# Kernel optimization log

Hardware: AMD Instinct MI355X
Metric: run time of the kernel (lower is better)

The kernel has to match this reference:

```python
import jax, jax.numpy as jnp
import numpy as np

EPSILON = 0.01  # from init_kwargs

def setup_inputs() -> dict:
    key = jax.random.key(0)
    k1, k2, k3, k4 = jax.random.split(key, 4)
    N, E, D = 100000, 3200000, 4
    x = jax.random.normal(k1, (N, D), dtype=jnp.float32)
    edge_index = jax.random.randint(k2, (2, E), 0, N, dtype=jnp.int32)
    boo_values = jax.random.normal(k3, (E, D, D), dtype=jnp.float32)
    mask = jnp.ones((N, 1), dtype=jnp.float32)
    diag = jax.random.uniform(k4, (N, D), dtype=jnp.float32)
    return {"x": x, "edge_index": edge_index, "boo_values": boo_values,
            "mask": mask, "diag": diag}

def reference(x, edge_index, boo_values, mask, diag):
    # y = eps*diag*x + A @ (diag * (A^T @ x)), A blocked-sparse with
    # per-edge blocks A_{row,col} = boo_values[e] in R^{DxD}.
    N = x.shape[0]
    row, col = edge_index[0], edge_index[1]
    # spmv_t (A^T x): gather x at row i, message A_ij^T x_i, scatter-add to col j
    msg_t = jnp.einsum('eji,ej->ei', boo_values, x[row])  # [E, D]
    AT_x = jax.ops.segment_sum(msg_t, col, num_segments=N) * mask  # [N, D]
    eps_x = EPSILON * x
    AT_x = AT_x * diag
    eps_x = eps_x * diag
    # spmv (A v): gather v at col j, message A_ij v_j, scatter-add to row i
    msg = jnp.einsum('eij,ej->ei', boo_values, AT_x[col])  # [E, D]
    A_AT_x = jax.ops.segment_sum(msg, row, num_segments=N) * mask  # [N, D]
    return eps_x + A_AT_x
```

## Files before the change

### kernel.cpp

```cpp
#include <hip/hip_runtime.h>

#define EPSILON 0.01f

#define BLK    256
#define SLICE  1024
#define SLOG   10
#define PCH    20
#define BCH    2048
#define MAXS   128


__global__ void init_cursors(int* cur1, int* cur2, int S, int cap) {
    int t = threadIdx.x;
    if (t < S) { cur1[t] = t * cap; cur2[t] = t * cap; }
}

__global__ void __launch_bounds__(BLK) bin_kernel(
    const int* __restrict__ row, const int* __restrict__ col,
    int2* __restrict__ bins1, int2* __restrict__ bins2,
    int* __restrict__ cur1, int* __restrict__ cur2,
    long long E, int S)
{
    __shared__ int2 st[BCH];
    __shared__ unsigned char ss[BCH];
    __shared__ int hist[MAXS], rnk[MAXS], sbase[MAXS], gbase[MAXS];
    const int t = threadIdx.x;

    long long start = (long long)blockIdx.x * BCH;
    long long endl  = start + BCH; if (endl > E) endl = E;
    const int cnt = (int)(endl - start);

    for (int side = 0; side < 2; ++side) {
        const int* __restrict__ key = side ? row : col;
        const int* __restrict__ oth = side ? col : row;
        int2* __restrict__ bins = side ? bins2 : bins1;
        int*  __restrict__ cur  = side ? cur2  : cur1;

        if (t < MAXS) { hist[t] = 0; rnk[t] = 0; }
        __syncthreads();

        for (int i0 = t * 4; i0 < cnt; i0 += BLK * 4) {
            if (i0 + 4 <= cnt) {
                int4 k = *reinterpret_cast<const int4*>(key + start + i0);
                atomicAdd(&hist[k.x >> SLOG], 1);
                atomicAdd(&hist[k.y >> SLOG], 1);
                atomicAdd(&hist[k.z >> SLOG], 1);
                atomicAdd(&hist[k.w >> SLOG], 1);
            } else {
                for (int i = i0; i < cnt; ++i)
                    atomicAdd(&hist[key[start + i] >> SLOG], 1);
            }
        }
        __syncthreads();

        if (t == 0) {
            int run = 0;
            for (int s2 = 0; s2 < S; ++s2) { sbase[s2] = run; run += hist[s2]; }
        }
        if (t < S) gbase[t] = atomicAdd(&cur[t], hist[t]);
        __syncthreads();

        for (int i0 = t * 4; i0 < cnt; i0 += BLK * 4) {
            if (i0 + 4 <= cnt) {
                int4 k = *reinterpret_cast<const int4*>(key + start + i0);
                int4 o = *reinterpret_cast<const int4*>(oth + start + i0);
                int kk[4] = {k.x, k.y, k.z, k.w};
                int oo[4] = {o.x, o.y, o.z, o.w};
                #pragma unroll
                for (int u = 0; u < 4; ++u) {
                    int s2 = kk[u] >> SLOG;
                    int slot = sbase[s2] + atomicAdd(&rnk[s2], 1);
                    st[slot] = make_int2((int)(start + i0 + u),
                                         ((kk[u] & (SLICE - 1)) << 17) | oo[u]);
                    ss[slot] = (unsigned char)s2;
                }
            } else {
                for (int i = i0; i < cnt; ++i) {
                    int kv = key[start + i], ov = oth[start + i];
                    int s2 = kv >> SLOG;
                    int slot = sbase[s2] + atomicAdd(&rnk[s2], 1);
                    st[slot] = make_int2((int)(start + i),
                                         ((kv & (SLICE - 1)) << 17) | ov);
                    ss[slot] = (unsigned char)s2;
                }
            }
        }
        __syncthreads();

        for (int i = t; i < cnt; i += BLK) {
            int s2 = ss[i];
            bins[(size_t)gbase[s2] + (i - sbase[s2])] = st[i];
        }
        __syncthreads();
    }
}

template<int PASS>
__global__ void __launch_bounds__(BLK) pass_kernel(
    const float4* __restrict__ boo,
    const int2*   __restrict__ bins,
    const int*    __restrict__ cur,
    const float4* __restrict__ src,
    float*        __restrict__ stage,
    int N, int cap, int P)
{
    __shared__ float acc[SLICE * 4];

    const int s    = blockIdx.x / P;
    const int p    = blockIdx.x - s * P;
    const int base = s << SLOG;
    const int lim  = min(SLICE, N - base);

    for (int i = threadIdx.x; i < SLICE * 4; i += BLK) acc[i] = 0.0f;
    __syncthreads();

    const int cnt = cur[s] - s * cap;
    const int lo  = (int)((long long)cnt * p / P);
    const int hi  = (int)((long long)cnt * (p + 1) / P);
    const int2* __restrict__ bin = bins + (size_t)s * cap;

    const int j  = (int)(threadIdx.x & 3);
    const int g0 = (int)(threadIdx.x >> 2);

    auto process = [&](int2 rec, float4 b) {
        float4 v = src[rec.y & 0x1FFFF];
        int loc = ((unsigned)rec.y) >> 17;
        float val;
        if (PASS == 2) {
            val = b.x * v.x + b.y * v.y + b.z * v.z + b.w * v.w;
        } else {
            float xj = (j == 0) ? v.x : (j == 1) ? v.y : (j == 2) ? v.z : v.w;
            float4 q;
            q.x = b.x * xj; q.y = b.y * xj; q.z = b.z * xj; q.w = b.w * xj;
            q.x += __shfl_xor(q.x, 1); q.y += __shfl_xor(q.y, 1);
            q.z += __shfl_xor(q.z, 1); q.w += __shfl_xor(q.w, 1);
            q.x += __shfl_xor(q.x, 2); q.y += __shfl_xor(q.y, 2);
            q.z += __shfl_xor(q.z, 2); q.w += __shfl_xor(q.w, 2);
            val = (j == 0) ? q.x : (j == 1) ? q.y : (j == 2) ? q.z : q.w;
        }
        atomicAdd(&acc[loc * 4 + j], val);
    };

    int i = lo + g0;
    for (; i + 64 < hi; i += 128) {
        int2 ra = bin[i];
        int2 rb = bin[i + 64];
        float4 ba = boo[(long long)ra.x * 4 + j];
        float4 bb = boo[(long long)rb.x * 4 + j];
        process(ra, ba);
        process(rb, bb);
    }
    if (i < hi) {
        int2 ra = bin[i];
        float4 ba = boo[(long long)ra.x * 4 + j];
        process(ra, ba);
    }
    __syncthreads();

    float* stg = stage + (size_t)blockIdx.x * (SLICE * 4);
    for (int f = threadIdx.x; f < lim * 4; f += BLK) stg[f] = acc[f];
}

__global__ void __launch_bounds__(BLK) mid_staged_kernel(
    const float4* __restrict__ stage,
    const float4* __restrict__ d4,
    const float*  __restrict__ mask,
    float4* __restrict__ v4,
    int N, int P)
{
    int n = blockIdx.x * BLK + threadIdx.x;
    if (n >= N) return;
    int s = n >> SLOG, local = n & (SLICE - 1);
    const float4* t = stage + ((size_t)s * P) * SLICE + local;
    float4 a = make_float4(0.f, 0.f, 0.f, 0.f);
    for (int p = 0; p < P; ++p) {
        float4 u = t[(size_t)p * SLICE];
        a.x += u.x; a.y += u.y; a.z += u.z; a.w += u.w;
    }
    float4 dv = d4[n];
    float  m  = mask[n];
    a.x *= dv.x * m; a.y *= dv.y * m; a.z *= dv.z * m; a.w *= dv.w * m;
    v4[n] = a;
}

__global__ void __launch_bounds__(BLK) fin_staged_kernel(
    const float4* __restrict__ stage,
    const float4* __restrict__ x4,
    const float4* __restrict__ d4,
    const float*  __restrict__ mask,
    float4* __restrict__ out4,
    int N, int P)
{
    int n = blockIdx.x * BLK + threadIdx.x;
    if (n >= N) return;
    int s = n >> SLOG, local = n & (SLICE - 1);
    const float4* t = stage + ((size_t)s * P) * SLICE + local;
    float4 a = make_float4(0.f, 0.f, 0.f, 0.f);
    for (int p = 0; p < P; ++p) {
        float4 u = t[(size_t)p * SLICE];
        a.x += u.x; a.y += u.y; a.z += u.z; a.w += u.w;
    }
    float4 xv = x4[n];
    float4 dv = d4[n];
    float  m  = mask[n];
    float4 o;
    o.x = EPSILON * xv.x * dv.x + a.x * m;
    o.y = EPSILON * xv.y * dv.y + a.y * m;
    o.z = EPSILON * xv.z * dv.z + a.z * m;
    o.w = EPSILON * xv.w * dv.w + a.w * m;
    out4[n] = o;
}

__global__ void __launch_bounds__(BLK) mid_atomic_kernel(
    const float4* __restrict__ x4,
    const float4* __restrict__ d4,
    const float*  __restrict__ mask,
    float4* __restrict__ atx,
    float4* __restrict__ out4,
    int N)
{
    int n = blockIdx.x * BLK + threadIdx.x;
    if (n >= N) return;
    float4 a  = atx[n];
    float4 dv = d4[n];
    float  m  = mask[n];
    a.x *= dv.x * m; a.y *= dv.y * m; a.z *= dv.z * m; a.w *= dv.w * m;
    atx[n] = a;
    float4 xv = x4[n];
    float4 o;
    o.x = EPSILON * xv.x * dv.x; o.y = EPSILON * xv.y * dv.y;
    o.z = EPSILON * xv.z * dv.z; o.w = EPSILON * xv.w * dv.w;
    out4[n] = o;
}

__global__ void __launch_bounds__(256) spmvt_kernel(
    const float4* __restrict__ boo, const int* __restrict__ row,
    const int* __restrict__ col, const float* __restrict__ x,
    float* __restrict__ ATx, long long E)
{
    long long t = (long long)blockIdx.x * blockDim.x + threadIdx.x;
    long long e = t >> 2;
    int j = (int)(t & 3);
    if (e >= E) return;
    float4 b = boo[e * 4 + j];
    int r = row[e];
    float xj = x[r * 4 + j];
    float4 p;
    p.x = b.x * xj; p.y = b.y * xj; p.z = b.z * xj; p.w = b.w * xj;
    p.x += __shfl_xor(p.x, 1); p.y += __shfl_xor(p.y, 1);
    p.z += __shfl_xor(p.z, 1); p.w += __shfl_xor(p.w, 1);
    p.x += __shfl_xor(p.x, 2); p.y += __shfl_xor(p.y, 2);
    p.z += __shfl_xor(p.z, 2); p.w += __shfl_xor(p.w, 2);
    float v = (j == 0) ? p.x : (j == 1) ? p.y : (j == 2) ? p.z : p.w;
    int c = col[e];
    unsafeAtomicAdd(&ATx[c * 4 + j], v);
}

__global__ void __launch_bounds__(256) spmv_kernel(
    const float4* __restrict__ boo, const int* __restrict__ row,
    const int* __restrict__ col, const float* __restrict__ vv,
    const float* __restrict__ mask, float* __restrict__ out, long long E)
{
    long long t = (long long)blockIdx.x * blockDim.x + threadIdx.x;
    long long e = t >> 2;
    int i = (int)(t & 3);
    if (e >= E) return;
    float4 b = boo[e * 4 + i];
    int c = col[e];
    const float4* v4 = (const float4*)vv;
    float4 v = v4[c];
    float mi = b.x * v.x + b.y * v.y + b.z * v.z + b.w * v.w;
    int r = row[e];
    float mr = mask[r];
    unsafeAtomicAdd(&out[r * 4 + i], mi * mr);
}

extern "C" void kernel_launch(void* const* d_in, const int* in_sizes, int n_in,
                              void* d_out, int out_size, void* d_ws, size_t ws_size,
                              hipStream_t stream) {
    const float* x    = (const float*)d_in[0];
    const int*   ei   = (const int*)d_in[1];
    const float* boo  = (const float*)d_in[2];
    const float* mask = (const float*)d_in[3];
    const float* diag = (const float*)d_in[4];
    float* out = (float*)d_out;

    int N = in_sizes[0] / 4;
    long long E = in_sizes[1] / 2;
    const int* row = ei;
    const int* col = ei + E;

    int S = (N + SLICE - 1) >> SLOG;
    int cap = (int)((E + S - 1) / S);
    cap += cap * 3 / 10;
    cap = (cap + 255) & ~255;

    size_t o_v   = 0;
    size_t o_cur = ((size_t)N * 16 + 255) & ~(size_t)255;
    size_t o_b1  = o_cur + 2048;
    size_t szb   = (size_t)S * cap * 8;
    size_t o_b2  = o_b1 + szb;
    size_t o_st  = o_b2 + szb;
    size_t szst  = (size_t)S * PCH * SLICE * 16;

    bool ok   = (S <= MAXS) && (N <= (1 << 17));
    int  tier = (!ok) ? 2 : (ws_size >= o_st + szst) ? 1 : 2;

    float* v    = (float*)((char*)d_ws + o_v);
    int*   cur1 = (int*)((char*)d_ws + o_cur);
    int*   cur2 = cur1 + 256;

    const int gNode = (N + BLK - 1) / BLK;
    const int gBin  = (int)((E + BCH - 1) / BCH);
    const int gPass = S * PCH;

    if (tier == 1) {
        int2*  bins1 = (int2*)((char*)d_ws + o_b1);
        int2*  bins2 = (int2*)((char*)d_ws + o_b2);
        float* stage = (float*)((char*)d_ws + o_st);

        init_cursors<<<1, MAXS, 0, stream>>>(cur1, cur2, S, cap);
        bin_kernel<<<gBin, BLK, 0, stream>>>(row, col, bins1, bins2, cur1, cur2, E, S);
        pass_kernel<1><<<gPass, BLK, 0, stream>>>(
            (const float4*)boo, bins1, cur1, (const float4*)x, stage, N, cap, PCH);
        mid_staged_kernel<<<gNode, BLK, 0, stream>>>(
            (const float4*)stage, (const float4*)diag, mask, (float4*)v, N, PCH);
        pass_kernel<2><<<gPass, BLK, 0, stream>>>(
            (const float4*)boo, bins2, cur2, (const float4*)v, stage, N, cap, PCH);
        fin_staged_kernel<<<gNode, BLK, 0, stream>>>(
            (const float4*)stage, (const float4*)x, (const float4*)diag, mask,
            (float4*)out, N, PCH);
    } else {
        hipMemsetAsync(v, 0, (size_t)N * 16, stream);
        long long T = E * 4;
        int gEdge = (int)((T + BLK - 1) / BLK);
        spmvt_kernel<<<gEdge, BLK, 0, stream>>>(
            (const float4*)boo, row, col, x, v, E);
        mid_atomic_kernel<<<gNode, BLK, 0, stream>>>(
            (const float4*)x, (const float4*)diag, mask, (float4*)v, (float4*)out, N);
        spmv_kernel<<<gEdge, BLK, 0, stream>>>(
            (const float4*)boo, row, col, v, mask, out, E);
    }
}
```

Baseline: 531.4 us.

## Use atomic scatter for first SpMV pass and bin only the second pass

The fast path now bins edges only by row, for the second A·v pass. The first A^T·x pass switches to the edge-parallel global-atomic scatter kernel followed by the atomic mid kernel, replacing the binned pass, its staging buffer and the staged reduction. This removes one binning sweep, one bins buffer and one staged reduction, at the cost of global float atomics across the node array in pass one. The binning chunk size also doubles to 4096 edges per block.

```diff
diff --git a/kernel.cpp b/kernel.cpp
--- a/kernel.cpp
+++ b/kernel.cpp
@@ -6,19 +6,18 @@
 #define SLICE  1024
 #define SLOG   10
 #define PCH    20
-#define BCH    2048
+#define BCH    4096
 #define MAXS   128
 
 
-__global__ void init_cursors(int* cur1, int* cur2, int S, int cap) {
+__global__ void init_cur(int* cur, int S, int cap) {
     int t = threadIdx.x;
-    if (t < S) { cur1[t] = t * cap; cur2[t] = t * cap; }
-}
-
-__global__ void __launch_bounds__(BLK) bin_kernel(
-    const int* __restrict__ row, const int* __restrict__ col,
-    int2* __restrict__ bins1, int2* __restrict__ bins2,
-    int* __restrict__ cur1, int* __restrict__ cur2,
+    if (t < S) cur[t] = t * cap;
+}
+
+__global__ void __launch_bounds__(BLK) bin1_kernel(
+    const int* __restrict__ key, const int* __restrict__ oth,
+    int2* __restrict__ bins, int* __restrict__ cur,
     long long E, int S)
 {
     __shared__ int2 st[BCH];
@@ -30,73 +29,64 @@
     long long endl  = start + BCH; if (endl > E) endl = E;
     const int cnt = (int)(endl - start);
 
-    for (int side = 0; side < 2; ++side) {
-        const int* __restrict__ key = side ? row : col;
-        const int* __restrict__ oth = side ? col : row;
-        int2* __restrict__ bins = side ? bins2 : bins1;
-        int*  __restrict__ cur  = side ? cur2  : cur1;
-
-        if (t < MAXS) { hist[t] = 0; rnk[t] = 0; }
-        __syncthreads();
-
-        for (int i0 = t * 4; i0 < cnt; i0 += BLK * 4) {
-            if (i0 + 4 <= cnt) {
-                int4 k = *reinterpret_cast<const int4*>(key + start + i0);
-                atomicAdd(&hist[k.x >> SLOG], 1);
-                atomicAdd(&hist[k.y >> SLOG], 1);
-                atomicAdd(&hist[k.z >> SLOG], 1);
-                atomicAdd(&hist[k.w >> SLOG], 1);
-            } else {
-                for (int i = i0; i < cnt; ++i)
-                    atomicAdd(&hist[key[start + i] >> SLOG], 1);
+    if (t < MAXS) { hist[t] = 0; rnk[t] = 0; }
+    __syncthreads();
+
+    for (int i0 = t * 4; i0 < cnt; i0 += BLK * 4) {
+        if (i0 + 4 <= cnt) {
+            int4 k = *reinterpret_cast<const int4*>(key + start + i0);
+            atomicAdd(&hist[k.x >> SLOG], 1);
+            atomicAdd(&hist[k.y >> SLOG], 1);
+            atomicAdd(&hist[k.z >> SLOG], 1);
+            atomicAdd(&hist[k.w >> SLOG], 1);
+        } else {
+            for (int i = i0; i < cnt; ++i)
+                atomicAdd(&hist[key[start + i] >> SLOG], 1);
+        }
+    }
+    __syncthreads();
+
+    if (t == 0) {
+        int run = 0;
+        for (int s2 = 0; s2 < S; ++s2) { sbase[s2] = run; run += hist[s2]; }
+    }
+    if (t < S) gbase[t] = atomicAdd(&cur[t], hist[t]);
+    __syncthreads();
+
+    for (int i0 = t * 4; i0 < cnt; i0 += BLK * 4) {
+        if (i0 + 4 <= cnt) {
+            int4 k = *reinterpret_cast<const int4*>(key + start + i0);
+            int4 o = *reinterpret_cast<const int4*>(oth + start + i0);
+            int kk[4] = {k.x, k.y, k.z, k.w};
+            int oo[4] = {o.x, o.y, o.z, o.w};
+            #pragma unroll
+            for (int u = 0; u < 4; ++u) {
+                int s2 = kk[u] >> SLOG;
+                int slot = sbase[s2] + atomicAdd(&rnk[s2], 1);
+                st[slot] = make_int2((int)(start + i0 + u),
+                                     ((kk[u] & (SLICE - 1)) << 17) | oo[u]);
+                ss[slot] = (unsigned char)s2;
+            }
+        } else {
+            for (int i = i0; i < cnt; ++i) {
+                int kv = key[start + i], ov = oth[start + i];
+                int s2 = kv >> SLOG;
+                int slot = sbase[s2] + atomicAdd(&rnk[s2], 1);
+                st[slot] = make_int2((int)(start + i),
+                                     ((kv & (SLICE - 1)) << 17) | ov);
+                ss[slot] = (unsigned char)s2;
             }
         }
-        __syncthreads();
-
-        if (t == 0) {
-            int run = 0;
-            for (int s2 = 0; s2 < S; ++s2) { sbase[s2] = run; run += hist[s2]; }
-        }
-        if (t < S) gbase[t] = atomicAdd(&cur[t], hist[t]);
-        __syncthreads();
-
-        for (int i0 = t * 4; i0 < cnt; i0 += BLK * 4) {
-            if (i0 + 4 <= cnt) {
-                int4 k = *reinterpret_cast<const int4*>(key + start + i0);
-                int4 o = *reinterpret_cast<const int4*>(oth + start + i0);
-                int kk[4] = {k.x, k.y, k.z, k.w};
-                int oo[4] = {o.x, o.y, o.z, o.w};
-                #pragma unroll
-                for (int u = 0; u < 4; ++u) {
-                    int s2 = kk[u] >> SLOG;
-                    int slot = sbase[s2] + atomicAdd(&rnk[s2], 1);
-                    st[slot] = make_int2((int)(start + i0 + u),
-                                         ((kk[u] & (SLICE - 1)) << 17) | oo[u]);
-                    ss[slot] = (unsigned char)s2;
-                }
-            } else {
-                for (int i = i0; i < cnt; ++i) {
-                    int kv = key[start + i], ov = oth[start + i];
-                    int s2 = kv >> SLOG;
-                    int slot = sbase[s2] + atomicAdd(&rnk[s2], 1);
-                    st[slot] = make_int2((int)(start + i),
-                                         ((kv & (SLICE - 1)) << 17) | ov);
-                    ss[slot] = (unsigned char)s2;
-                }
-            }
-        }
-        __syncthreads();
-
-        for (int i = t; i < cnt; i += BLK) {
-            int s2 = ss[i];
-            bins[(size_t)gbase[s2] + (i - sbase[s2])] = st[i];
-        }
-        __syncthreads();
-    }
-}
-
-template<int PASS>
-__global__ void __launch_bounds__(BLK) pass_kernel(
+    }
+    __syncthreads();
+
+    for (int i = t; i < cnt; i += BLK) {
+        int s2 = ss[i];
+        bins[(size_t)gbase[s2] + (i - sbase[s2])] = st[i];
+    }
+}
+
+__global__ void __launch_bounds__(BLK) pass2_kernel(
     const float4* __restrict__ boo,
     const int2*   __restrict__ bins,
     const int*    __restrict__ cur,
@@ -125,19 +115,7 @@
     auto process = [&](int2 rec, float4 b) {
         float4 v = src[rec.y & 0x1FFFF];
         int loc = ((unsigned)rec.y) >> 17;
-        float val;
-        if (PASS == 2) {
-            val = b.x * v.x + b.y * v.y + b.z * v.z + b.w * v.w;
-        } else {
-            float xj = (j == 0) ? v.x : (j == 1) ? v.y : (j == 2) ? v.z : v.w;
-            float4 q;
-            q.x = b.x * xj; q.y = b.y * xj; q.z = b.z * xj; q.w = b.w * xj;
-            q.x += __shfl_xor(q.x, 1); q.y += __shfl_xor(q.y, 1);
-            q.z += __shfl_xor(q.z, 1); q.w += __shfl_xor(q.w, 1);
-            q.x += __shfl_xor(q.x, 2); q.y += __shfl_xor(q.y, 2);
-            q.z += __shfl_xor(q.z, 2); q.w += __shfl_xor(q.w, 2);
-            val = (j == 0) ? q.x : (j == 1) ? q.y : (j == 2) ? q.z : q.w;
-        }
+        float val = b.x * v.x + b.y * v.y + b.z * v.z + b.w * v.w;
         atomicAdd(&acc[loc * 4 + j], val);
     };
 
@@ -159,28 +137,6 @@
 
     float* stg = stage + (size_t)blockIdx.x * (SLICE * 4);
     for (int f = threadIdx.x; f < lim * 4; f += BLK) stg[f] = acc[f];
-}
-
-__global__ void __launch_bounds__(BLK) mid_staged_kernel(
-    const float4* __restrict__ stage,
-    const float4* __restrict__ d4,
-    const float*  __restrict__ mask,
-    float4* __restrict__ v4,
-    int N, int P)
-{
-    int n = blockIdx.x * BLK + threadIdx.x;
-    if (n >= N) return;
-    int s = n >> SLOG, local = n & (SLICE - 1);
-    const float4* t = stage + ((size_t)s * P) * SLICE + local;
-    float4 a = make_float4(0.f, 0.f, 0.f, 0.f);
-    for (int p = 0; p < P; ++p) {
-        float4 u = t[(size_t)p * SLICE];
-        a.x += u.x; a.y += u.y; a.z += u.z; a.w += u.w;
-    }
-    float4 dv = d4[n];
-    float  m  = mask[n];
-    a.x *= dv.x * m; a.y *= dv.y * m; a.z *= dv.z * m; a.w *= dv.w * m;
-    v4[n] = a;
 }
 
 __global__ void __launch_bounds__(BLK) fin_staged_kernel(
@@ -297,9 +253,8 @@
 
     size_t o_v   = 0;
     size_t o_cur = ((size_t)N * 16 + 255) & ~(size_t)255;
-    size_t o_b1  = o_cur + 2048;
+    size_t o_b2  = o_cur + 2048;
     size_t szb   = (size_t)S * cap * 8;
-    size_t o_b2  = o_b1 + szb;
     size_t o_st  = o_b2 + szb;
     size_t szst  = (size_t)S * PCH * SLICE * 16;
 
@@ -307,33 +262,32 @@
     int  tier = (!ok) ? 2 : (ws_size >= o_st + szst) ? 1 : 2;
 
     float* v    = (float*)((char*)d_ws + o_v);
-    int*   cur1 = (int*)((char*)d_ws + o_cur);
-    int*   cur2 = cur1 + 256;
+    int*   cur2 = (int*)((char*)d_ws + o_cur);
 
     const int gNode = (N + BLK - 1) / BLK;
     const int gBin  = (int)((E + BCH - 1) / BCH);
     const int gPass = S * PCH;
+    long long T = E * 4;
+    const int gEdge = (int)((T + BLK - 1) / BLK);
+
+    hipMemsetAsync(v, 0, (size_t)N * 16, stream);
 
     if (tier == 1) {
-        int2*  bins1 = (int2*)((char*)d_ws + o_b1);
         int2*  bins2 = (int2*)((char*)d_ws + o_b2);
         float* stage = (float*)((char*)d_ws + o_st);
 
-        init_cursors<<<1, MAXS, 0, stream>>>(cur1, cur2, S, cap);
-        bin_kernel<<<gBin, BLK, 0, stream>>>(row, col, bins1, bins2, cur1, cur2, E, S);
-        pass_kernel<1><<<gPass, BLK, 0, stream>>>(
-            (const float4*)boo, bins1, cur1, (const float4*)x, stage, N, cap, PCH);
-        mid_staged_kernel<<<gNode, BLK, 0, stream>>>(
-            (const float4*)stage, (const float4*)diag, mask, (float4*)v, N, PCH);
-        pass_kernel<2><<<gPass, BLK, 0, stream>>>(
+        init_cur<<<1, MAXS, 0, stream>>>(cur2, S, cap);
+        bin1_kernel<<<gBin, BLK, 0, stream>>>(row, col, bins2, cur2, E, S);
+        spmvt_kernel<<<gEdge, BLK, 0, stream>>>(
+            (const float4*)boo, row, col, x, v, E);
+        mid_atomic_kernel<<<gNode, BLK, 0, stream>>>(
+            (const float4*)x, (const float4*)diag, mask, (float4*)v, (float4*)out, N);
+        pass2_kernel<<<gPass, BLK, 0, stream>>>(
             (const float4*)boo, bins2, cur2, (const float4*)v, stage, N, cap, PCH);
         fin_staged_kernel<<<gNode, BLK, 0, stream>>>(
             (const float4*)stage, (const float4*)x, (const float4*)diag, mask,
             (float4*)out, N, PCH);
     } else {
-        hipMemsetAsync(v, 0, (size_t)N * 16, stream);
-        long long T = E * 4;
-        int gEdge = (int)((T + BLK - 1) / BLK);
         spmvt_kernel<<<gEdge, BLK, 0, stream>>>(
             (const float4*)boo, row, col, x, v, E);
         mid_atomic_kernel<<<gNode, BLK, 0, stream>>>(
```

New measurement: 510.9 us. 1.04x faster.
